# Optimization experiments

Hardware: AMD Instinct MI355X
Metric: run time of the kernel (lower is better)

## Reference

```python
import jax, jax.numpy as jnp
import numpy as np
import math

B, S, D, H = 2, 2048, 1024, 16
DH = D // H
MASK_VALUE = -1000000.0  # module uses -1e6, not -inf


def setup_inputs() -> dict:
    key = jax.random.key(0)
    ks = jax.random.split(key, 8)
    scale = 1.0 / math.sqrt(D)
    return {
        "queries": jax.random.normal(ks[0], (B, S, D), jnp.float32),
        "keys": jax.random.normal(ks[1], (B, S, D), jnp.float32),
        "values": jax.random.normal(ks[2], (B, S, D), jnp.float32),
        "valid_lens": jax.random.randint(ks[3], (B,), 1, S + 1, jnp.int32),
        "Wq": jax.random.normal(ks[4], (D, D), jnp.float32) * scale,
        "Wk": jax.random.normal(ks[5], (D, D), jnp.float32) * scale,
        "Wv": jax.random.normal(ks[6], (D, D), jnp.float32) * scale,
        "Wo": jax.random.normal(ks[7], (D, D), jnp.float32) * scale,
    }


def _split_heads(x):
    # [B, S, D] -> [B, H, S, DH]
    b, s, d = x.shape
    return x.reshape(b, s, H, DH).transpose(0, 2, 1, 3)


def reference(queries, keys, values, valid_lens, Wq, Wk, Wv, Wo):
    q = _split_heads(queries @ Wq)          # [B, H, S, DH]
    k = _split_heads(keys @ Wk)
    v = _split_heads(values @ Wv)
    scores = jnp.einsum("bhqd,bhkd->bhqk", q, k) / math.sqrt(DH)
    # valid_lens [B]: one length per batch row, broadcast over heads & queries
    mask = jnp.arange(scores.shape[-1])[None, None, None, :] < valid_lens[:, None, None, None]
    scores = jnp.where(mask, scores, MASK_VALUE)
    attn = jax.nn.softmax(scores, axis=-1)  # dropout is identity in eval
    out = jnp.einsum("bhqk,bhkd->bhqd", attn, v)   # [B, H, S, DH]
    out = out.transpose(0, 2, 1, 3).reshape(queries.shape[0], queries.shape[1], D)
    return out @ Wo
```

## Files before the change

### kernel.cpp

```cpp
#include <hip/hip_runtime.h>
#include <stdint.h>

#define BB 2
#define SS 2048
#define DD 1024
#define HH 16
#define DHD 64
#define MM (BB * SS)

typedef unsigned short u16;
typedef unsigned int u32;
typedef __attribute__((ext_vector_type(8))) short bhalf8;
typedef __attribute__((ext_vector_type(4))) float floatx4;
typedef __attribute__((ext_vector_type(2))) u32 u32x2;
typedef __attribute__((address_space(3))) u32 as3_u32;
typedef __attribute__((address_space(1))) u32 as1_u32;

__device__ __forceinline__ u16 f2bf(float f) {
  u32 u = __float_as_uint(f);
  u32 r = (u + 0x7FFFu + ((u >> 16) & 1u)) >> 16;
  return (u16)r;
}

__device__ __forceinline__ u32 cvtpk_bf16(float lo, float hi) {
  u32 r;
  asm("v_cvt_pk_bf16_f32 %0, %1, %2" : "=v"(r) : "v"(lo), "v"(hi));
  return r;
}

__device__ __forceinline__ float exp2_fast(float x) {
  float r;
  asm("v_exp_f32 %0, %1" : "=v"(r) : "v"(x));
  return r;
}

__device__ __forceinline__ void gload16(const void* g, const void* l) {
  __builtin_amdgcn_global_load_lds((as1_u32*)(uintptr_t)g, (as3_u32*)(uintptr_t)l, 16, 0, 0);
}

__global__ void k_convert3(const float* __restrict__ q, const float* __restrict__ k,
                           const float* __restrict__ v, u16* __restrict__ out) {
  const int z = blockIdx.y;
  const float* src = (z == 0) ? q : (z == 1) ? k : v;
  const int i = blockIdx.x * 256 + threadIdx.x;
  float4 val = ((const float4*)src)[i];
  ushort4 o;
  o.x = f2bf(val.x); o.y = f2bf(val.y); o.z = f2bf(val.z); o.w = f2bf(val.w);
  ((ushort4*)(out + (size_t)z * 4194304))[i] = o;
}

__global__ void k_transpose4(const float* __restrict__ Wq, const float* __restrict__ Wk,
                             const float* __restrict__ Wv, const float* __restrict__ Wo,
                             u16* __restrict__ Wt) {
  const int z = blockIdx.z;
  const float* W = (z == 0) ? Wq : (z == 1) ? Wk : (z == 2) ? Wv : Wo;
  const float sc = (z == 0) ? 0.18033688011112042f : 1.0f;
  __shared__ u16 tile[32][33];
  const int tx = threadIdx.x, ty = threadIdx.y;
  const int n0 = blockIdx.x * 32, k0 = blockIdx.y * 32;
#pragma unroll
  for (int i = 0; i < 4; ++i)
    tile[ty + 8 * i][tx] = f2bf(W[(size_t)(k0 + ty + 8 * i) * DD + n0 + tx] * sc);
  __syncthreads();
  u16* dst = Wt + (size_t)z * 1048576;
#pragma unroll
  for (int i = 0; i < 4; ++i)
    dst[(size_t)(n0 + ty + 8 * i) * DD + k0 + tx] = tile[tx][ty + 8 * i];
}

__global__ __launch_bounds__(256, 2) void k_gemm_qkv(
    const u16* __restrict__ Xq, const u16* __restrict__ Xk, const u16* __restrict__ Xv,
    const u16* __restrict__ Wt, u16* __restrict__ Qb, u16* __restrict__ Kb,
    u16* __restrict__ Vtb) {
  const int id = blockIdx.x;
  const int rr = id & 7, t8 = id >> 3;
  const int g = (t8 >> 3) * 8 + rr, c = t8 & 7;
  const int z = g / 32, by = g % 32, bx = c;
  const u16* A = (z == 0) ? Xq : (z == 1) ? Xk : Xv;
  const u16* Bt = Wt + (size_t)z * 1048576;
  __shared__ __attribute__((aligned(16))) u16 sA[2][128 * 32];
  __shared__ __attribute__((aligned(16))) u16 sB[2][128 * 32];
  const int t = threadIdx.x;
  const int w = t >> 6, lane = t & 63;
  const int lr = lane & 15, lg = lane >> 4;
  const int wr = w >> 1, wc = w & 1;
  const int row0 = by * 128, col0 = bx * 128;

  const int srow = t >> 2;
  const int skoff = (t & 3) * 8;
  const u16* gA = A + (size_t)(row0 + srow) * DD + skoff;
  const u16* gB = Bt + (size_t)(col0 + srow) * DD + skoff;
  const int ldsbase = w * 512;

  floatx4 acc[4][4] = {};

  auto stage = [&](int buf, int kt) {
    const int ko = kt * 32;
    gload16(gA + ko, &sA[buf][ldsbase]);
    gload16(gA + ko + (size_t)64 * DD, &sA[buf][2048 + ldsbase]);
    gload16(gB + ko, &sB[buf][ldsbase]);
    gload16(gB + ko + (size_t)64 * DD, &sB[buf][2048 + ldsbase]);
  };

  int cur = 0;
  stage(0, 0);
  __syncthreads();
  for (int kt = 0; kt < 32; ++kt) {
    if (kt + 1 < 32) stage(cur ^ 1, kt + 1);
    bhalf8 af[4], bf[4];
#pragma unroll
    for (int m = 0; m < 4; ++m)
      af[m] = *(const bhalf8*)&sA[cur][(wr * 64 + m * 16 + lr) * 32 + lg * 8];
#pragma unroll
    for (int n = 0; n < 4; ++n)
      bf[n] = *(const bhalf8*)&sB[cur][(wc * 64 + n * 16 + lr) * 32 + lg * 8];
#pragma unroll
    for (int m = 0; m < 4; ++m)
#pragma unroll
      for (int n = 0; n < 4; ++n)
        acc[m][n] = __builtin_amdgcn_mfma_f32_16x16x32_bf16(af[m], bf[n], acc[m][n], 0, 0, 0);
    __syncthreads();
    cur ^= 1;
  }

#pragma unroll
  for (int m = 0; m < 4; ++m) {
#pragma unroll
    for (int n = 0; n < 4; ++n) {
      const int col = col0 + wc * 64 + n * 16 + lr;
      const int rowb = row0 + wr * 64 + m * 16 + lg * 4;
      if (z == 2) {
        const int bidx = rowb >> 11, s = rowb & (SS - 1);
        ushort4 pk;
        pk.x = f2bf(acc[m][n][0]); pk.y = f2bf(acc[m][n][1]);
        pk.z = f2bf(acc[m][n][2]); pk.w = f2bf(acc[m][n][3]);
        *(ushort4*)&Vtb[((size_t)bidx * 1024 + col) * SS + s] = pk;
      } else {
        u16* C = (z == 0) ? Qb : Kb;
#pragma unroll
        for (int r = 0; r < 4; ++r)
          C[(size_t)(rowb + r) * DD + col] = f2bf(acc[m][n][r]);
      }
    }
  }
}

__global__ __launch_bounds__(256, 2) void k_gemm_wo(
    const u16* __restrict__ A, const u16* __restrict__ Bt, float* __restrict__ C) {
  const int id = blockIdx.x;
  const int rr = id & 7, t8 = id >> 3;
  const int g = (t8 >> 3) * 8 + rr, c = t8 & 7;
  const int by = g, bx = c;
  __shared__ __attribute__((aligned(16))) u16 sA[2][64 * 32];
  __shared__ __attribute__((aligned(16))) u16 sB[2][128 * 32];
  const int t = threadIdx.x;
  const int w = t >> 6, lane = t & 63;
  const int lr = lane & 15, lg = lane >> 4;
  const int wr = w >> 1, wc = w & 1;
  const int row0 = by * 64, col0 = bx * 128;

  const int srow = t >> 2;
  const int skoff = (t & 3) * 8;
  const u16* gA = A + (size_t)(row0 + srow) * DD + skoff;
  const u16* gB = Bt + (size_t)(col0 + srow) * DD + skoff;
  const int ldsbase = w * 512;

  floatx4 acc[2][4] = {};

  auto stage = [&](int buf, int kt) {
    const int ko = kt * 32;
    gload16(gA + ko, &sA[buf][ldsbase]);
    gload16(gB + ko, &sB[buf][ldsbase]);
    gload16(gB + ko + (size_t)64 * DD, &sB[buf][2048 + ldsbase]);
  };

  int cur = 0;
  stage(0, 0);
  __syncthreads();
  for (int kt = 0; kt < 32; ++kt) {
    if (kt + 1 < 32) stage(cur ^ 1, kt + 1);
    bhalf8 af[2], bf[4];
#pragma unroll
    for (int m = 0; m < 2; ++m)
      af[m] = *(const bhalf8*)&sA[cur][(wr * 32 + m * 16 + lr) * 32 + lg * 8];
#pragma unroll
    for (int n = 0; n < 4; ++n)
      bf[n] = *(const bhalf8*)&sB[cur][(wc * 64 + n * 16 + lr) * 32 + lg * 8];
#pragma unroll
    for (int m = 0; m < 2; ++m)
#pragma unroll
      for (int n = 0; n < 4; ++n)
        acc[m][n] = __builtin_amdgcn_mfma_f32_16x16x32_bf16(af[m], bf[n], acc[m][n], 0, 0, 0);
    __syncthreads();
    cur ^= 1;
  }

#pragma unroll
  for (int m = 0; m < 2; ++m)
#pragma unroll
    for (int n = 0; n < 4; ++n) {
      const int col = col0 + wc * 64 + n * 16 + lr;
      const int rowb = row0 + wr * 32 + m * 16 + lg * 4;
#pragma unroll
      for (int r = 0; r < 4; ++r)
        C[(size_t)(rowb + r) * DD + col] = acc[m][n][r];
    }
}

__global__ __launch_bounds__(256, 2) void k_attn(
    const u16* __restrict__ Q, const u16* __restrict__ K, const u16* __restrict__ Vt,
    float* __restrict__ Opart, float2* __restrict__ Ml,
    const int* __restrict__ valid_lens, const int part) {
  const int id = blockIdx.x;
  const int rr = id & 7, tt = id >> 3;
  const int g = (tt >> 5) * 8 + rr, c = tt & 31;
  const int h = g & 15, zi = g >> 4;
  const int b = zi & 1, p = zi >> 1;
  const int t = threadIdx.x;
  const int w = t >> 6, lane = t & 63;
  const int lr = lane & 15, lg = lane >> 4;
  const int q0 = c * 64 + w * 16;
  const int vl = valid_lens[b];
  const int kbeg = p * part;
  if (kbeg >= vl) return;
  const int kend = (vl < kbeg + part) ? vl : (kbeg + part);
  const int L = kend - kbeg;

  __shared__ __attribute__((aligned(16))) u16 kbuf[2][64 * 64];
  __shared__ __attribute__((aligned(16))) u16 vbuf[2][64 * 64];
  __shared__ __attribute__((aligned(16))) u16 p_lds[4][16 * 72];
  u16* pl = &p_lds[w][0];

  const u16* Qp = Q + ((size_t)(b * SS + q0 + lr)) * DD + h * DHD;
  const bhalf8 qf0 = *(const bhalf8*)(Qp + lg * 8);
  const bhalf8 qf1 = *(const bhalf8*)(Qp + 32 + lg * 8);

  const int sub = lane >> 3;
  const int sc16 = (lane & 7) ^ sub;
  const u16* ksrc = K + (size_t)(b * SS + kbeg + w * 16 + sub) * DD + h * DHD + sc16 * 8;
  const u16* vsrc = Vt + ((size_t)(b * HH + h) * DHD + w * 16 + sub) * SS + kbeg + sc16 * 8;

  auto stage = [&](int buf, int i) {
    const int sk0 = i * 64;
    gload16(ksrc + (size_t)sk0 * DD,       &kbuf[buf][(w * 16) * 64]);
    gload16(ksrc + (size_t)(sk0 + 8) * DD, &kbuf[buf][(w * 16 + 8) * 64]);
    gload16(vsrc + sk0,                    &vbuf[buf][(w * 16) * 64]);
    gload16(vsrc + (size_t)8 * SS + sk0,   &vbuf[buf][(w * 16 + 8) * 64]);
  };

  float mrun = -1e30f, lrun = 0.f;
  floatx4 o[4] = {};

  const int nblk = (L + 63) >> 6;
  const bool partial = (L & 63) != 0;
  const int swz = lr & 7;

  stage(0, 0);
  __syncthreads();

  int cb = 0;
  for (int i = 0; i < nblk; ++i) {
    if (i + 1 < nblk) stage(cb ^ 1, i + 1);
    const u16* kb = &kbuf[cb][0];
    const u16* vb = &vbuf[cb][0];
    floatx4 s[4];
    __builtin_amdgcn_s_setprio(1);
#pragma unroll
    for (int cc = 0; cc < 4; ++cc) {
      const bhalf8 kc0 = *(const bhalf8*)&kb[(cc * 16 + lr) * 64 + ((lg ^ swz) * 8)];
      const bhalf8 kc1 = *(const bhalf8*)&kb[(cc * 16 + lr) * 64 + (((lg + 4) ^ swz) * 8)];
      floatx4 zz = {0.f, 0.f, 0.f, 0.f};
      zz = __builtin_amdgcn_mfma_f32_16x16x32_bf16(kc0, qf0, zz, 0, 0, 0);
      s[cc] = __builtin_amdgcn_mfma_f32_16x16x32_bf16(kc1, qf1, zz, 0, 0, 0);
    }
    __builtin_amdgcn_s_setprio(0);
    if (partial && i == nblk - 1) {
      const int sk0 = i * 64;
#pragma unroll
      for (int cc = 0; cc < 4; ++cc)
#pragma unroll
        for (int r = 0; r < 4; ++r)
          if (sk0 + cc * 16 + lg * 4 + r >= L) s[cc][r] = -1e6f;
    }
    float tmax = fmaxf(fmaxf(fmaxf(s[0][0], s[0][1]), fmaxf(s[0][2], s[0][3])),
                       fmaxf(fmaxf(s[1][0], s[1][1]), fmaxf(s[1][2], s[1][3])));
    tmax = fmaxf(tmax, fmaxf(fmaxf(fmaxf(s[2][0], s[2][1]), fmaxf(s[2][2], s[2][3])),
                             fmaxf(fmaxf(s[3][0], s[3][1]), fmaxf(s[3][2], s[3][3]))));
    tmax = fmaxf(tmax, __shfl_xor(tmax, 16));
    tmax = fmaxf(tmax, __shfl_xor(tmax, 32));
    if (!__all(tmax <= mrun + 8.0f)) {
      const float nm = fmaxf(mrun, tmax);
      const float sc = exp2_fast(mrun - nm);
      mrun = nm;
      lrun *= sc;
      float scb[4];
#pragma unroll
      for (int r = 0; r < 4; ++r) scb[r] = __shfl(sc, lg * 4 + r);
#pragma unroll
      for (int dt = 0; dt < 4; ++dt)
#pragma unroll
        for (int r = 0; r < 4; ++r) o[dt][r] *= scb[r];
    }
    float rs = 0.f;
    u32 pk[4][2];
#pragma unroll
    for (int cc = 0; cc < 4; ++cc) {
      float p0 = exp2_fast(s[cc][0] - mrun), p1 = exp2_fast(s[cc][1] - mrun);
      float p2 = exp2_fast(s[cc][2] - mrun), p3 = exp2_fast(s[cc][3] - mrun);
      rs += (p0 + p1) + (p2 + p3);
      pk[cc][0] = cvtpk_bf16(p0, p1);
      pk[cc][1] = cvtpk_bf16(p2, p3);
    }
    rs += __shfl_xor(rs, 16);
    rs += __shfl_xor(rs, 32);
    lrun += rs;
#pragma unroll
    for (int cc = 0; cc < 4; ++cc) {
      u32x2 pr; pr.x = pk[cc][0]; pr.y = pk[cc][1];
      *(u32x2*)&pl[lr * 72 + cc * 16 + lg * 4] = pr;
    }
    asm volatile("s_waitcnt lgkmcnt(0)" ::: "memory");
    const bhalf8 pa0 = *(const bhalf8*)&pl[lr * 72 + lg * 8];
    const bhalf8 pa1 = *(const bhalf8*)&pl[lr * 72 + 32 + lg * 8];
    __builtin_amdgcn_s_setprio(1);
#pragma unroll
    for (int dt = 0; dt < 4; ++dt) {
      const bhalf8 vf0 = *(const bhalf8*)&vb[(dt * 16 + lr) * 64 + ((lg ^ swz) * 8)];
      const bhalf8 vf1 = *(const bhalf8*)&vb[(dt * 16 + lr) * 64 + (((lg + 4) ^ swz) * 8)];
      o[dt] = __builtin_amdgcn_mfma_f32_16x16x32_bf16(pa0, vf0, o[dt], 0, 0, 0);
      o[dt] = __builtin_amdgcn_mfma_f32_16x16x32_bf16(pa1, vf1, o[dt], 0, 0, 0);
    }
    __builtin_amdgcn_s_setprio(0);
    __syncthreads();
    cb ^= 1;
  }

  const size_t rowbase = ((size_t)(b * HH + h)) * SS + q0;
  const size_t pbase = (size_t)p * (BB * HH * SS);
#pragma unroll
  for (int dt = 0; dt < 4; ++dt)
#pragma unroll
    for (int r = 0; r < 4; ++r)
      Opart[(pbase + rowbase + lg * 4 + r) * DHD + dt * 16 + lr] = o[dt][r];
  if (lane < 16) {
    float2 ml; ml.x = mrun; ml.y = lrun;
    Ml[pbase + rowbase + lr] = ml;
  }
}

template <int P>
__global__ void k_merge(const float* __restrict__ Opart, const float2* __restrict__ Ml,
                        const int* __restrict__ valid_lens, u16* __restrict__ Ob) {
  const int t = threadIdx.x;
  const int rid = blockIdx.x * 16 + (t >> 4);
  const int dc = t & 15;
  const int b = rid >> 15;
  const int h = (rid >> 11) & (HH - 1);
  const int s = rid & (SS - 1);
  const int vl = valid_lens[b];
  constexpr int part = SS / P;
  float m[P], l[P];
  float4 o4[P];
  bool live[P];
  float M = -1e30f;
#pragma unroll
  for (int p = 0; p < P; ++p) {
    live[p] = (p * part < vl);
    if (live[p]) {
      float2 ml = Ml[(size_t)p * (BB * HH * SS) + rid];
      m[p] = ml.x; l[p] = ml.y;
      o4[p] = *(const float4*)&Opart[((size_t)p * (BB * HH * SS) + rid) * DHD + dc * 4];
      M = fmaxf(M, m[p]);
    }
  }
  float L = 0.f;
  float4 acc = {0.f, 0.f, 0.f, 0.f};
#pragma unroll
  for (int p = 0; p < P; ++p)
    if (live[p]) {
      const float wgt = exp2_fast(m[p] - M);
      L += l[p] * wgt;
      acc.x += wgt * o4[p].x; acc.y += wgt * o4[p].y;
      acc.z += wgt * o4[p].z; acc.w += wgt * o4[p].w;
    }
  const float inv = 1.0f / L;
  ushort4 r;
  r.x = f2bf(acc.x * inv); r.y = f2bf(acc.y * inv);
  r.z = f2bf(acc.z * inv); r.w = f2bf(acc.w * inv);
  *(ushort4*)&Ob[((size_t)(b * SS + s)) * DD + h * DHD + dc * 4] = r;
}

extern "C" void kernel_launch(void* const* d_in, const int* in_sizes, int n_in,
                              void* d_out, int out_size, void* d_ws, size_t ws_size,
                              hipStream_t stream) {
  const float* q = (const float*)d_in[0];
  const float* k = (const float*)d_in[1];
  const float* v = (const float*)d_in[2];
  const int* vl = (const int*)d_in[3];
  const float* Wq = (const float*)d_in[4];
  const float* Wk = (const float*)d_in[5];
  const float* Wv = (const float*)d_in[6];
  const float* Wo = (const float*)d_in[7];

  char* ws = (char*)d_ws;
  u16* Xq  = (u16*)(ws + 0);
  u16* Wtq = (u16*)(ws + 25165824);
  u16* Wto = (u16*)(ws + 31457280);
  u16* Qb  = (u16*)(ws + 33554432);
  u16* Kb  = (u16*)(ws + 41943040);
  u16* Vtb = (u16*)(ws + 50331648);
  u16* Ob  = (u16*)(ws + 58720256);

  const bool big = ws_size >= (size_t)134 * 1024 * 1024;
  const int P = big ? 2 : 1;
  const int part = SS / P;
  float* Opart = big ? (float*)(ws + 67108864) : (float*)(ws + 0);
  float2* Ml   = big ? (float2*)(ws + 67108864 + (size_t)2 * BB * HH * SS * DHD * 4)
                     : (float2*)(ws + 16777216);

  k_convert3<<<dim3(4096, 3), 256, 0, stream>>>(q, k, v, Xq);
  k_transpose4<<<dim3(32, 32, 4), dim3(32, 8), 0, stream>>>(Wq, Wk, Wv, Wo, Wtq);
  k_gemm_qkv<<<768, 256, 0, stream>>>(Xq, Xq + 4194304, Xq + 8388608, Wtq, Qb, Kb, Vtb);
  k_attn<<<1024 * P, 256, 0, stream>>>(Qb, Kb, Vtb, Opart, Ml, vl, part);
  if (big) k_merge<2><<<4096, 256, 0, stream>>>(Opart, Ml, vl, Ob);
  else     k_merge<1><<<4096, 256, 0, stream>>>(Opart, Ml, vl, Ob);
  k_gemm_wo<<<512, 256, 0, stream>>>(Ob, Wto, (float*)d_out);
}
```

Baseline: 205.5 us.

## Fuse input bf16 conversion into QKV GEMM and split-merge into output GEMM

Drops the standalone fp32-to-bf16 conversion kernel: the QKV GEMM now loads fp32 activations into LDS with an XOR swizzle and converts them to bf16 when building MFMA fragments. It also drops the separate merge kernel: the Wo GEMM reads the partial attention outputs and softmax statistics directly, combines the splits, normalises, and writes bf16 tiles into LDS inside its main loop. This removes two launches and the round trips through the bf16 intermediates in global memory. In exchange, the QKV GEMM uses twice the LDS for the A tile and adds conversion work in its inner loop, and the Wo GEMM now does register-staged, non-async A loads plus merge arithmetic inside the K loop.

```diff
diff --git a/kernel.cpp b/kernel.cpp
--- a/kernel.cpp
+++ b/kernel.cpp
@@ -13,6 +13,7 @@
 typedef __attribute__((ext_vector_type(8))) short bhalf8;
 typedef __attribute__((ext_vector_type(4))) float floatx4;
 typedef __attribute__((ext_vector_type(2))) u32 u32x2;
+typedef __attribute__((ext_vector_type(4))) u32 u32x4;
 typedef __attribute__((address_space(3))) u32 as3_u32;
 typedef __attribute__((address_space(1))) u32 as1_u32;
 
@@ -36,17 +37,6 @@
 
 __device__ __forceinline__ void gload16(const void* g, const void* l) {
   __builtin_amdgcn_global_load_lds((as1_u32*)(uintptr_t)g, (as3_u32*)(uintptr_t)l, 16, 0, 0);
-}
-
-__global__ void k_convert3(const float* __restrict__ q, const float* __restrict__ k,
-                           const float* __restrict__ v, u16* __restrict__ out) {
-  const int z = blockIdx.y;
-  const float* src = (z == 0) ? q : (z == 1) ? k : v;
-  const int i = blockIdx.x * 256 + threadIdx.x;
-  float4 val = ((const float4*)src)[i];
-  ushort4 o;
-  o.x = f2bf(val.x); o.y = f2bf(val.y); o.z = f2bf(val.z); o.w = f2bf(val.w);
-  ((ushort4*)(out + (size_t)z * 4194304))[i] = o;
 }
 
 __global__ void k_transpose4(const float* __restrict__ Wq, const float* __restrict__ Wk,
@@ -69,16 +59,16 @@
 }
 
 __global__ __launch_bounds__(256, 2) void k_gemm_qkv(
-    const u16* __restrict__ Xq, const u16* __restrict__ Xk, const u16* __restrict__ Xv,
+    const float* __restrict__ Xq, const float* __restrict__ Xk, const float* __restrict__ Xv,
     const u16* __restrict__ Wt, u16* __restrict__ Qb, u16* __restrict__ Kb,
     u16* __restrict__ Vtb) {
   const int id = blockIdx.x;
   const int rr = id & 7, t8 = id >> 3;
   const int g = (t8 >> 3) * 8 + rr, c = t8 & 7;
   const int z = g / 32, by = g % 32, bx = c;
-  const u16* A = (z == 0) ? Xq : (z == 1) ? Xk : Xv;
+  const float* A = (z == 0) ? Xq : (z == 1) ? Xk : Xv;
   const u16* Bt = Wt + (size_t)z * 1048576;
-  __shared__ __attribute__((aligned(16))) u16 sA[2][128 * 32];
+  __shared__ __attribute__((aligned(16))) float sAf[2][128 * 32];
   __shared__ __attribute__((aligned(16))) u16 sB[2][128 * 32];
   const int t = threadIdx.x;
   const int w = t >> 6, lane = t & 63;
@@ -86,22 +76,25 @@
   const int wr = w >> 1, wc = w & 1;
   const int row0 = by * 128, col0 = bx * 128;
 
-  const int srow = t >> 2;
-  const int skoff = (t & 3) * 8;
-  const u16* gA = A + (size_t)(row0 + srow) * DD + skoff;
-  const u16* gB = Bt + (size_t)(col0 + srow) * DD + skoff;
-  const int ldsbase = w * 512;
+  const int scol16 = (lane & 7) ^ (lane >> 3);
+  const float* gA0 = A + (size_t)(row0 + w * 8 + (lane >> 3)) * DD + scol16 * 4;
+  const int srowB = t >> 2;
+  const int skoffB = (t & 3) * 8;
+  const u16* gB = Bt + (size_t)(col0 + srowB) * DD + skoffB;
+  const int ldsbaseB = w * 512;
 
   floatx4 acc[4][4] = {};
 
   auto stage = [&](int buf, int kt) {
     const int ko = kt * 32;
-    gload16(gA + ko, &sA[buf][ldsbase]);
-    gload16(gA + ko + (size_t)64 * DD, &sA[buf][2048 + ldsbase]);
-    gload16(gB + ko, &sB[buf][ldsbase]);
-    gload16(gB + ko + (size_t)64 * DD, &sB[buf][2048 + ldsbase]);
+#pragma unroll
+    for (int j = 0; j < 4; ++j)
+      gload16(gA0 + (size_t)j * 32 * DD + ko, &sAf[buf][w * 256 + j * 1024]);
+    gload16(gB + ko, &sB[buf][ldsbaseB]);
+    gload16(gB + ko + (size_t)64 * DD, &sB[buf][2048 + ldsbaseB]);
   };
 
+  const int swz = lr & 7;
   int cur = 0;
   stage(0, 0);
   __syncthreads();
@@ -109,8 +102,15 @@
     if (kt + 1 < 32) stage(cur ^ 1, kt + 1);
     bhalf8 af[4], bf[4];
 #pragma unroll
-    for (int m = 0; m < 4; ++m)
-      af[m] = *(const bhalf8*)&sA[cur][(wr * 64 + m * 16 + lr) * 32 + lg * 8];
+    for (int m = 0; m < 4; ++m) {
+      const int r = wr * 64 + m * 16 + lr;
+      const float4 a0 = *(const float4*)&sAf[cur][(r * 8 + ((lg * 2) ^ swz)) * 4];
+      const float4 a1 = *(const float4*)&sAf[cur][(r * 8 + ((lg * 2 + 1) ^ swz)) * 4];
+      u32x4 pk;
+      pk.x = cvtpk_bf16(a0.x, a0.y); pk.y = cvtpk_bf16(a0.z, a0.w);
+      pk.z = cvtpk_bf16(a1.x, a1.y); pk.w = cvtpk_bf16(a1.z, a1.w);
+      af[m] = __builtin_bit_cast(bhalf8, pk);
+    }
 #pragma unroll
     for (int n = 0; n < 4; ++n)
       bf[n] = *(const bhalf8*)&sB[cur][(wc * 64 + n * 16 + lr) * 32 + lg * 8];
@@ -145,8 +145,11 @@
   }
 }
 
+template <int P>
 __global__ __launch_bounds__(256, 2) void k_gemm_wo(
-    const u16* __restrict__ A, const u16* __restrict__ Bt, float* __restrict__ C) {
+    const float* __restrict__ Opart, const float2* __restrict__ Ml,
+    const int* __restrict__ valid_lens, const u16* __restrict__ Bt,
+    float* __restrict__ C) {
   const int id = blockIdx.x;
   const int rr = id & 7, t8 = id >> 3;
   const int g = (t8 >> 3) * 8 + rr, c = t8 & 7;
@@ -159,26 +162,75 @@
   const int wr = w >> 1, wc = w & 1;
   const int row0 = by * 64, col0 = bx * 128;
 
-  const int srow = t >> 2;
-  const int skoff = (t & 3) * 8;
-  const u16* gA = A + (size_t)(row0 + srow) * DD + skoff;
-  const u16* gB = Bt + (size_t)(col0 + srow) * DD + skoff;
-  const int ldsbase = w * 512;
+  const int arow = t >> 2;
+  const int R = row0 + arow;
+  const int bb = R >> 11, s = R & (SS - 1);
+  const int dcol = (t & 3) * 8;
+  const bool live1 = (P == 2) && (valid_lens[bb] > SS / P);
+  constexpr size_t PSTRIDE = (size_t)BB * HH * SS;
+
+  const int srowB = t >> 2;
+  const int skoffB = (t & 3) * 8;
+  const u16* gB = Bt + (size_t)(col0 + srowB) * DD + skoffB;
+  const int ldsbaseB = w * 512;
 
   floatx4 acc[2][4] = {};
-
-  auto stage = [&](int buf, int kt) {
+  float4 x0, x1, y0, y1;
+  float w0, w1;
+
+  auto loadA = [&](int kt) {
+    const int hh = kt >> 1, d0 = (kt & 1) * 32 + dcol;
+    const size_t rbase = (size_t)(bb * HH + hh) * SS + s;
+    x0 = *(const float4*)&Opart[rbase * DHD + d0];
+    x1 = *(const float4*)&Opart[rbase * DHD + d0 + 4];
+    const float2 ml0 = Ml[rbase];
+    float L;
+    if (live1) {
+      const float2 ml1 = Ml[PSTRIDE + rbase];
+      y0 = *(const float4*)&Opart[(PSTRIDE + rbase) * DHD + d0];
+      y1 = *(const float4*)&Opart[(PSTRIDE + rbase) * DHD + d0 + 4];
+      const float M = fmaxf(ml0.x, ml1.x);
+      w0 = exp2_fast(ml0.x - M);
+      w1 = exp2_fast(ml1.x - M);
+      L = ml0.y * w0 + ml1.y * w1;
+    } else {
+      w0 = 1.f; w1 = 0.f;
+      L = ml0.y;
+    }
+    const float inv = 1.0f / L;
+    w0 *= inv; w1 *= inv;
+  };
+
+  auto writeA = [&](int buf) {
+    float f0 = x0.x * w0, f1 = x0.y * w0, f2 = x0.z * w0, f3 = x0.w * w0;
+    float f4 = x1.x * w0, f5 = x1.y * w0, f6 = x1.z * w0, f7 = x1.w * w0;
+    if (live1) {
+      f0 += y0.x * w1; f1 += y0.y * w1; f2 += y0.z * w1; f3 += y0.w * w1;
+      f4 += y1.x * w1; f5 += y1.y * w1; f6 += y1.z * w1; f7 += y1.w * w1;
+    }
+    u32x4 pk;
+    pk.x = cvtpk_bf16(f0, f1); pk.y = cvtpk_bf16(f2, f3);
+    pk.z = cvtpk_bf16(f4, f5); pk.w = cvtpk_bf16(f6, f7);
+    *(u32x4*)&sA[buf][arow * 32 + (t & 3) * 8] = pk;
+  };
+
+  auto stageB = [&](int buf, int kt) {
     const int ko = kt * 32;
-    gload16(gA + ko, &sA[buf][ldsbase]);
-    gload16(gB + ko, &sB[buf][ldsbase]);
-    gload16(gB + ko + (size_t)64 * DD, &sB[buf][2048 + ldsbase]);
+    gload16(gB + ko, &sB[buf][ldsbaseB]);
+    gload16(gB + ko + (size_t)64 * DD, &sB[buf][2048 + ldsbaseB]);
   };
 
+  loadA(0);
+  stageB(0, 0);
+  writeA(0);
+  __syncthreads();
+
   int cur = 0;
-  stage(0, 0);
-  __syncthreads();
   for (int kt = 0; kt < 32; ++kt) {
-    if (kt + 1 < 32) stage(cur ^ 1, kt + 1);
+    if (kt + 1 < 32) {
+      stageB(cur ^ 1, kt + 1);
+      loadA(kt + 1);
+    }
     bhalf8 af[2], bf[4];
 #pragma unroll
     for (int m = 0; m < 2; ++m)
@@ -191,6 +243,7 @@
 #pragma unroll
       for (int n = 0; n < 4; ++n)
         acc[m][n] = __builtin_amdgcn_mfma_f32_16x16x32_bf16(af[m], bf[n], acc[m][n], 0, 0, 0);
+    if (kt + 1 < 32) writeA(cur ^ 1);
     __syncthreads();
     cur ^= 1;
   }
@@ -348,48 +401,6 @@
   }
 }
 
-template <int P>
-__global__ void k_merge(const float* __restrict__ Opart, const float2* __restrict__ Ml,
-                        const int* __restrict__ valid_lens, u16* __restrict__ Ob) {
-  const int t = threadIdx.x;
-  const int rid = blockIdx.x * 16 + (t >> 4);
-  const int dc = t & 15;
-  const int b = rid >> 15;
-  const int h = (rid >> 11) & (HH - 1);
-  const int s = rid & (SS - 1);
-  const int vl = valid_lens[b];
-  constexpr int part = SS / P;
-  float m[P], l[P];
-  float4 o4[P];
-  bool live[P];
-  float M = -1e30f;
-#pragma unroll
-  for (int p = 0; p < P; ++p) {
-    live[p] = (p * part < vl);
-    if (live[p]) {
-      float2 ml = Ml[(size_t)p * (BB * HH * SS) + rid];
-      m[p] = ml.x; l[p] = ml.y;
-      o4[p] = *(const float4*)&Opart[((size_t)p * (BB * HH * SS) + rid) * DHD + dc * 4];
-      M = fmaxf(M, m[p]);
-    }
-  }
-  float L = 0.f;
-  float4 acc = {0.f, 0.f, 0.f, 0.f};
-#pragma unroll
-  for (int p = 0; p < P; ++p)
-    if (live[p]) {
-      const float wgt = exp2_fast(m[p] - M);
-      L += l[p] * wgt;
-      acc.x += wgt * o4[p].x; acc.y += wgt * o4[p].y;
-      acc.z += wgt * o4[p].z; acc.w += wgt * o4[p].w;
-    }
-  const float inv = 1.0f / L;
-  ushort4 r;
-  r.x = f2bf(acc.x * inv); r.y = f2bf(acc.y * inv);
-  r.z = f2bf(acc.z * inv); r.w = f2bf(acc.w * inv);
-  *(ushort4*)&Ob[((size_t)(b * SS + s)) * DD + h * DHD + dc * 4] = r;
-}
-
 extern "C" void kernel_launch(void* const* d_in, const int* in_sizes, int n_in,
                               void* d_out, int out_size, void* d_ws, size_t ws_size,
                               hipStream_t stream) {
@@ -403,26 +414,21 @@
   const float* Wo = (const float*)d_in[7];
 
   char* ws = (char*)d_ws;
-  u16* Xq  = (u16*)(ws + 0);
-  u16* Wtq = (u16*)(ws + 25165824);
-  u16* Wto = (u16*)(ws + 31457280);
-  u16* Qb  = (u16*)(ws + 33554432);
-  u16* Kb  = (u16*)(ws + 41943040);
-  u16* Vtb = (u16*)(ws + 50331648);
-  u16* Ob  = (u16*)(ws + 58720256);
+  u16* Wt  = (u16*)(ws + 0);
+  u16* Qb  = (u16*)(ws + 8388608);
+  u16* Kb  = (u16*)(ws + 16777216);
+  u16* Vtb = (u16*)(ws + 25165824);
+  float* Opart = (float*)(ws + 33554432);
 
   const bool big = ws_size >= (size_t)134 * 1024 * 1024;
   const int P = big ? 2 : 1;
   const int part = SS / P;
-  float* Opart = big ? (float*)(ws + 67108864) : (float*)(ws + 0);
-  float2* Ml   = big ? (float2*)(ws + 67108864 + (size_t)2 * BB * HH * SS * DHD * 4)
-                     : (float2*)(ws + 16777216);
-
-  k_convert3<<<dim3(4096, 3), 256, 0, stream>>>(q, k, v, Xq);
-  k_transpose4<<<dim3(32, 32, 4), dim3(32, 8), 0, stream>>>(Wq, Wk, Wv, Wo, Wtq);
-  k_gemm_qkv<<<768, 256, 0, stream>>>(Xq, Xq + 4194304, Xq + 8388608, Wtq, Qb, Kb, Vtb);
+  float2* Ml = big ? (float2*)(ws + 67108864) : (float2*)(ws + 50331648);
+
+  k_transpose4<<<dim3(32, 32, 4), dim3(32, 8), 0, stream>>>(Wq, Wk, Wv, Wo, Wt);
+  k_gemm_qkv<<<768, 256, 0, stream>>>(q, k, v, Wt, Qb, Kb, Vtb);
   k_attn<<<1024 * P, 256, 0, stream>>>(Qb, Kb, Vtb, Opart, Ml, vl, part);
-  if (big) k_merge<2><<<4096, 256, 0, stream>>>(Opart, Ml, vl, Ob);
-  else     k_merge<1><<<4096, 256, 0, stream>>>(Opart, Ml, vl, Ob);
-  k_gemm_wo<<<512, 256, 0, stream>>>(Ob, Wto, (float*)d_out);
-}
+  u16* Wto = Wt + 3 * 1048576;
+  if (big) k_gemm_wo<2><<<512, 256, 0, stream>>>(Opart, Ml, vl, Wto, (float*)d_out);
+  else     k_gemm_wo<1><<<512, 256, 0, stream>>>(Opart, Ml, vl, Wto, (float*)d_out);
+}
```

After: 228.6 us. 11.2% more time.

## Fuse fp32-to-bf16 activation conversion into QKV GEMM and swizzle LDS tiles

Applied to the files above, without the earlier changes.

Drops the separate conversion kernel. The QKV GEMM now loads fp32 activations into registers, packs them to bf16 with v_cvt_pk_bf16_f32, and writes them to LDS after the MFMA step, overlapping that work with compute. LDS tiles in both GEMMs use an XOR swizzle on 16-byte units to reduce bank conflicts on fragment reads. Attention launch bounds are raised to 3 blocks per CU. In exchange, the A operand moves twice the global bytes per tile through registers, which adds VGPR pressure, and the higher occupancy target for attention may force register spills.

```diff
diff --git a/kernel.cpp b/kernel.cpp
--- a/kernel.cpp
+++ b/kernel.cpp
@@ -13,6 +13,7 @@
 typedef __attribute__((ext_vector_type(8))) short bhalf8;
 typedef __attribute__((ext_vector_type(4))) float floatx4;
 typedef __attribute__((ext_vector_type(2))) u32 u32x2;
+typedef __attribute__((ext_vector_type(4))) u32 u32x4;
 typedef __attribute__((address_space(3))) u32 as3_u32;
 typedef __attribute__((address_space(1))) u32 as1_u32;
 
@@ -36,17 +37,6 @@
 
 __device__ __forceinline__ void gload16(const void* g, const void* l) {
   __builtin_amdgcn_global_load_lds((as1_u32*)(uintptr_t)g, (as3_u32*)(uintptr_t)l, 16, 0, 0);
-}
-
-__global__ void k_convert3(const float* __restrict__ q, const float* __restrict__ k,
-                           const float* __restrict__ v, u16* __restrict__ out) {
-  const int z = blockIdx.y;
-  const float* src = (z == 0) ? q : (z == 1) ? k : v;
-  const int i = blockIdx.x * 256 + threadIdx.x;
-  float4 val = ((const float4*)src)[i];
-  ushort4 o;
-  o.x = f2bf(val.x); o.y = f2bf(val.y); o.z = f2bf(val.z); o.w = f2bf(val.w);
-  ((ushort4*)(out + (size_t)z * 4194304))[i] = o;
 }
 
 __global__ void k_transpose4(const float* __restrict__ Wq, const float* __restrict__ Wk,
@@ -69,14 +59,14 @@
 }
 
 __global__ __launch_bounds__(256, 2) void k_gemm_qkv(
-    const u16* __restrict__ Xq, const u16* __restrict__ Xk, const u16* __restrict__ Xv,
+    const float* __restrict__ Xq, const float* __restrict__ Xk, const float* __restrict__ Xv,
     const u16* __restrict__ Wt, u16* __restrict__ Qb, u16* __restrict__ Kb,
     u16* __restrict__ Vtb) {
   const int id = blockIdx.x;
   const int rr = id & 7, t8 = id >> 3;
   const int g = (t8 >> 3) * 8 + rr, c = t8 & 7;
   const int z = g / 32, by = g % 32, bx = c;
-  const u16* A = (z == 0) ? Xq : (z == 1) ? Xk : Xv;
+  const float* A = (z == 0) ? Xq : (z == 1) ? Xk : Xv;
   const u16* Bt = Wt + (size_t)z * 1048576;
   __shared__ __attribute__((aligned(16))) u16 sA[2][128 * 32];
   __shared__ __attribute__((aligned(16))) u16 sB[2][128 * 32];
@@ -86,39 +76,64 @@
   const int wr = w >> 1, wc = w & 1;
   const int row0 = by * 128, col0 = bx * 128;
 
+  const int arow = t >> 1, ahalf = t & 1;
+  const float* gA = A + (size_t)(row0 + arow) * DD + ahalf * 16;
+  const int aswz = arow & 3;
   const int srow = t >> 2;
-  const int skoff = (t & 3) * 8;
-  const u16* gA = A + (size_t)(row0 + srow) * DD + skoff;
-  const u16* gB = Bt + (size_t)(col0 + srow) * DD + skoff;
+  const int sunit = (t & 3) ^ (srow & 3);
+  const u16* gB = Bt + (size_t)(col0 + srow) * DD + sunit * 8;
   const int ldsbase = w * 512;
 
   floatx4 acc[4][4] = {};
-
-  auto stage = [&](int buf, int kt) {
+  float4 ar0, ar1, ar2, ar3;
+
+  auto loadA = [&](int kt) {
+    const float* p = gA + kt * 32;
+    ar0 = *(const float4*)(p);
+    ar1 = *(const float4*)(p + 4);
+    ar2 = *(const float4*)(p + 8);
+    ar3 = *(const float4*)(p + 12);
+  };
+  auto writeA = [&](int buf) {
+    u32x4 w0, w1;
+    w0.x = cvtpk_bf16(ar0.x, ar0.y); w0.y = cvtpk_bf16(ar0.z, ar0.w);
+    w0.z = cvtpk_bf16(ar1.x, ar1.y); w0.w = cvtpk_bf16(ar1.z, ar1.w);
+    w1.x = cvtpk_bf16(ar2.x, ar2.y); w1.y = cvtpk_bf16(ar2.z, ar2.w);
+    w1.z = cvtpk_bf16(ar3.x, ar3.y); w1.w = cvtpk_bf16(ar3.z, ar3.w);
+    *(u32x4*)&sA[buf][arow * 32 + ((ahalf * 2) ^ aswz) * 8] = w0;
+    *(u32x4*)&sA[buf][arow * 32 + ((ahalf * 2 + 1) ^ aswz) * 8] = w1;
+  };
+  auto stageB = [&](int buf, int kt) {
     const int ko = kt * 32;
-    gload16(gA + ko, &sA[buf][ldsbase]);
-    gload16(gA + ko + (size_t)64 * DD, &sA[buf][2048 + ldsbase]);
     gload16(gB + ko, &sB[buf][ldsbase]);
     gload16(gB + ko + (size_t)64 * DD, &sB[buf][2048 + ldsbase]);
   };
 
+  loadA(0);
+  stageB(0, 0);
+  writeA(0);
+  __syncthreads();
+
+  const int fswz = lr & 3;
   int cur = 0;
-  stage(0, 0);
-  __syncthreads();
   for (int kt = 0; kt < 32; ++kt) {
-    if (kt + 1 < 32) stage(cur ^ 1, kt + 1);
+    if (kt + 1 < 32) {
+      stageB(cur ^ 1, kt + 1);
+      loadA(kt + 1);
+    }
     bhalf8 af[4], bf[4];
 #pragma unroll
     for (int m = 0; m < 4; ++m)
-      af[m] = *(const bhalf8*)&sA[cur][(wr * 64 + m * 16 + lr) * 32 + lg * 8];
+      af[m] = *(const bhalf8*)&sA[cur][(wr * 64 + m * 16 + lr) * 32 + ((lg ^ fswz) * 8)];
 #pragma unroll
     for (int n = 0; n < 4; ++n)
-      bf[n] = *(const bhalf8*)&sB[cur][(wc * 64 + n * 16 + lr) * 32 + lg * 8];
+      bf[n] = *(const bhalf8*)&sB[cur][(wc * 64 + n * 16 + lr) * 32 + ((lg ^ fswz) * 8)];
 #pragma unroll
     for (int m = 0; m < 4; ++m)
 #pragma unroll
       for (int n = 0; n < 4; ++n)
         acc[m][n] = __builtin_amdgcn_mfma_f32_16x16x32_bf16(af[m], bf[n], acc[m][n], 0, 0, 0);
+    if (kt + 1 < 32) writeA(cur ^ 1);
     __syncthreads();
     cur ^= 1;
   }
@@ -160,9 +175,9 @@
   const int row0 = by * 64, col0 = bx * 128;
 
   const int srow = t >> 2;
-  const int skoff = (t & 3) * 8;
-  const u16* gA = A + (size_t)(row0 + srow) * DD + skoff;
-  const u16* gB = Bt + (size_t)(col0 + srow) * DD + skoff;
+  const int sunit = (t & 3) ^ (srow & 3);
+  const u16* gA = A + (size_t)(row0 + srow) * DD + sunit * 8;
+  const u16* gB = Bt + (size_t)(col0 + srow) * DD + sunit * 8;
   const int ldsbase = w * 512;
 
   floatx4 acc[2][4] = {};
@@ -174,6 +189,7 @@
     gload16(gB + ko + (size_t)64 * DD, &sB[buf][2048 + ldsbase]);
   };
 
+  const int fswz = lr & 3;
   int cur = 0;
   stage(0, 0);
   __syncthreads();
@@ -182,10 +198,10 @@
     bhalf8 af[2], bf[4];
 #pragma unroll
     for (int m = 0; m < 2; ++m)
-      af[m] = *(const bhalf8*)&sA[cur][(wr * 32 + m * 16 + lr) * 32 + lg * 8];
+      af[m] = *(const bhalf8*)&sA[cur][(wr * 32 + m * 16 + lr) * 32 + ((lg ^ fswz) * 8)];
 #pragma unroll
     for (int n = 0; n < 4; ++n)
-      bf[n] = *(const bhalf8*)&sB[cur][(wc * 64 + n * 16 + lr) * 32 + lg * 8];
+      bf[n] = *(const bhalf8*)&sB[cur][(wc * 64 + n * 16 + lr) * 32 + ((lg ^ fswz) * 8)];
 #pragma unroll
     for (int m = 0; m < 2; ++m)
 #pragma unroll
@@ -207,7 +223,7 @@
     }
 }
 
-__global__ __launch_bounds__(256, 2) void k_attn(
+__global__ __launch_bounds__(256, 3) void k_attn(
     const u16* __restrict__ Q, const u16* __restrict__ K, const u16* __restrict__ Vt,
     float* __restrict__ Opart, float2* __restrict__ Ml,
     const int* __restrict__ valid_lens, const int part) {
@@ -403,26 +419,23 @@
   const float* Wo = (const float*)d_in[7];
 
   char* ws = (char*)d_ws;
-  u16* Xq  = (u16*)(ws + 0);
-  u16* Wtq = (u16*)(ws + 25165824);
-  u16* Wto = (u16*)(ws + 31457280);
-  u16* Qb  = (u16*)(ws + 33554432);
-  u16* Kb  = (u16*)(ws + 41943040);
-  u16* Vtb = (u16*)(ws + 50331648);
-  u16* Ob  = (u16*)(ws + 58720256);
+  u16* Wt  = (u16*)(ws + 0);
+  u16* Qb  = (u16*)(ws + 8388608);
+  u16* Kb  = (u16*)(ws + 16777216);
+  u16* Vtb = (u16*)(ws + 25165824);
+  u16* Ob  = (u16*)(ws + 33554432);
 
   const bool big = ws_size >= (size_t)134 * 1024 * 1024;
   const int P = big ? 2 : 1;
   const int part = SS / P;
-  float* Opart = big ? (float*)(ws + 67108864) : (float*)(ws + 0);
-  float2* Ml   = big ? (float2*)(ws + 67108864 + (size_t)2 * BB * HH * SS * DHD * 4)
-                     : (float2*)(ws + 16777216);
-
-  k_convert3<<<dim3(4096, 3), 256, 0, stream>>>(q, k, v, Xq);
-  k_transpose4<<<dim3(32, 32, 4), dim3(32, 8), 0, stream>>>(Wq, Wk, Wv, Wo, Wtq);
-  k_gemm_qkv<<<768, 256, 0, stream>>>(Xq, Xq + 4194304, Xq + 8388608, Wtq, Qb, Kb, Vtb);
+  float* Opart = (float*)(ws + 50331648);
+  float2* Ml   = big ? (float2*)(ws + 92274688) : (float2*)(ws + 67108864);
+
+  k_transpose4<<<dim3(32, 32, 4), dim3(32, 8), 0, stream>>>(Wq, Wk, Wv, Wo, Wt);
+  k_gemm_qkv<<<768, 256, 0, stream>>>(q, k, v, Wt, Qb, Kb, Vtb);
   k_attn<<<1024 * P, 256, 0, stream>>>(Qb, Kb, Vtb, Opart, Ml, vl, part);
   if (big) k_merge<2><<<4096, 256, 0, stream>>>(Opart, Ml, vl, Ob);
   else     k_merge<1><<<4096, 256, 0, stream>>>(Opart, Ml, vl, Ob);
+  u16* Wto = Wt + 3 * 1048576;
   k_gemm_wo<<<512, 256, 0, stream>>>(Ob, Wto, (float*)d_out);
 }
```

Result: slower. 219.5 us (+6.8%).
